# Optimization experiments

Measured on AMD Instinct MI355X. Metric: run time of the kernel, lower is better.

## Reference

```python
import jax, jax.numpy as jnp
import numpy as np

NUM_USERS = 100000
NUM_ITEMS = 50000
N_NODES = NUM_USERS + NUM_ITEMS
N_EDGES = 2400000
EMB = 64
BATCH = 4096
GCN_LAYERS = 3
TAU = 0.2
SSL_LAMBDA = 0.1
REG_LAMBDA = 1e-4


def setup_inputs() -> dict:
    key = jax.random.key(0)
    ks = jax.random.split(key, 8)
    user = jax.random.randint(ks[0], (BATCH,), 0, NUM_USERS, dtype=jnp.int32)
    pos_item = jax.random.randint(ks[1], (BATCH,), 0, NUM_ITEMS, dtype=jnp.int32)
    neg_item = jax.random.randint(ks[2], (BATCH,), 0, NUM_ITEMS, dtype=jnp.int32)
    # symmetric bipartite edges: user -> item and item -> user
    half = N_EDGES // 2
    src_u = jax.random.randint(ks[3], (half,), 0, NUM_USERS, dtype=jnp.int32)
    dst_i = jax.random.randint(ks[4], (half,), NUM_USERS, N_NODES, dtype=jnp.int32)
    adj_row = jnp.concatenate([src_u, dst_i])
    adj_col = jnp.concatenate([dst_i, src_u])
    # normalized-adjacency-like small positive values
    adj_val = jax.random.uniform(ks[5], (N_EDGES,), dtype=jnp.float32) * 0.01
    user_emb_w = jax.random.normal(ks[6], (NUM_USERS, EMB), dtype=jnp.float32) * 0.1
    item_emb_w = jax.random.normal(ks[7], (NUM_ITEMS, EMB), dtype=jnp.float32) * 0.1
    return {"user": user, "pos_item": pos_item, "neg_item": neg_item,
            "adj_row": adj_row, "adj_col": adj_col, "adj_val": adj_val,
            "user_emb_w": user_emb_w, "item_emb_w": item_emb_w}


def _aggregate(adj_row, adj_col, adj_val, user_emb_w, item_emb_w):
    emb = jnp.concatenate([user_emb_w, item_emb_w], axis=0)  # [N, d]
    acc = emb
    e = emb
    for _ in range(GCN_LAYERS):
        # sparse.mm(adj, e): gather columns, scale, scatter-add into rows
        e = jax.ops.segment_sum(adj_val[:, None] * e[adj_col], adj_row,
                                num_segments=N_NODES)
        acc = acc + e
    final = acc / (GCN_LAYERS + 1)  # mean over stacked layer outputs
    return final[:NUM_USERS], final[NUM_USERS:]


def reference(user, pos_item, neg_item, adj_row, adj_col, adj_val,
              user_emb_w, item_emb_w):
    user_all, item_all = _aggregate(adj_row, adj_col, adj_val,
                                    user_emb_w, item_emb_w)
    u = user_all[user]          # [B, d]
    pos = item_all[pos_item]    # [B, d]
    neg = item_all[neg_item]    # [B, d]
    # BPR loss
    pos_s = jnp.sum(u * pos, axis=-1)
    neg_s = jnp.sum(u * neg, axis=-1)
    bpr_loss = -jnp.mean(jax.nn.log_sigmoid(pos_s - neg_s))
    # L2 regularization
    b = u.shape[0]
    reg_loss = 0.5 * (jnp.sum(u * u) + jnp.sum(pos * pos) + jnp.sum(neg * neg)) / b
    reg_loss = reg_loss * REG_LAMBDA
    # neighbor-aggregate SSL (InfoNCE between user and its positive item)
    un = u / jnp.linalg.norm(u, axis=-1, keepdims=True)
    pn = pos / jnp.linalg.norm(pos, axis=-1, keepdims=True)
    logits = un @ pn.T / TAU                       # [B, B]
    pos_logit = jnp.diagonal(logits)
    na_loss = jnp.mean(jax.nn.logsumexp(logits, axis=1) - pos_logit) * SSL_LAMBDA
    return bpr_loss + reg_loss + na_loss
```

## Files before the change

### kernel.cpp

```cpp
#include <hip/hip_runtime.h>
#include <hip/hip_fp16.h>
#include <math.h>

#define NUM_USERS 100000
#define NUM_ITEMS 50000
#define N_NODES   150000
#define N_EDGES   2400000
#define HALF_E    (N_EDGES / 2)
#define EMB       64
#define BATCH     4096
#define TAU        0.2f
#define SSL_LAMBDA 0.1f
#define REG_LAMBDA 1e-4f

#define NB        293
#define BROWS     512
#define CAP       13632
#define BINA_BLK  512
#define PER_BLK   ((HALF_E + BINA_BLK - 1) / BINA_BLK)
#define EBUF_CAP  (2 * PER_BLK)
#define CAST_BLK  9375

__device__ __forceinline__ float wave_sum(float v) {
    #pragma unroll
    for (int m = 1; m < 64; m <<= 1) v += __shfl_xor(v, m, 64);
    return v;
}
__device__ __forceinline__ __half2 bits2h2(int b) {
    union { int i; __half2 h; } u; u.i = b; return u.h;
}
__device__ __forceinline__ int h22bits(__half2 h) {
    union { int i; __half2 h; } u; u.h = h; return u.i;
}
__device__ __forceinline__ float h2f(unsigned short s) {
    union { unsigned short s; __half h; } u; u.s = s; return __half2float(u.h);
}
__device__ __forceinline__ unsigned short f2h_bits(float x) {
    union { __half h; unsigned short s; } u; u.h = __float2half_rn(x); return u.s;
}

__global__ __launch_bounds__(256) void prep_kernel(
        const float4* __restrict__ uw4, const float4* __restrict__ iw4,
        uint2* __restrict__ h,
        const int* __restrict__ row, const int* __restrict__ col,
        const float* __restrict__ val,
        int* __restrict__ bucket_cursor, int2* __restrict__ arena) {
    __shared__ int hist[NB];
    __shared__ int lbase[NB];
    __shared__ int delta[NB];
    __shared__ int sm[256];
    __shared__ int2 ebuf[EBUF_CAP];
    const int t = threadIdx.x;
    size_t i = (size_t)blockIdx.x * 256 + t;
    const size_t tot = (size_t)N_NODES * EMB / 4;
    if (i < tot) {
        const size_t nu = (size_t)NUM_USERS * EMB / 4;
        float4 v = (i < nu) ? uw4[i] : iw4[i - nu];
        h[i] = make_uint2(h22bits(__floats2half2_rn(v.x, v.y)),
                          h22bits(__floats2half2_rn(v.z, v.w)));
    }
    if (blockIdx.x >= BINA_BLK) return;
    for (int k = t; k < NB; k += 256) hist[k] = 0;
    __syncthreads();
    const int beg = blockIdx.x * PER_BLK;
    const int end = min(beg + PER_BLK, HALF_E);
    for (int e = beg + t; e < end; e += 256) {
        int r = row[e], c = col[e];
        atomicAdd(&hist[r >> 9], 1);
        atomicAdd(&hist[c >> 9], 1);
    }
    __syncthreads();
    int v0 = (2 * t < NB) ? hist[2 * t] : 0;
    int v1 = (2 * t + 1 < NB) ? hist[2 * t + 1] : 0;
    int s = v0 + v1;
    sm[t] = s;
    __syncthreads();
    for (int m = 1; m < 256; m <<= 1) {
        int y = (t >= m) ? sm[t - m] : 0;
        __syncthreads();
        sm[t] += y;
        __syncthreads();
    }
    int excl = sm[t] - s;
    if (2 * t < NB) lbase[2 * t] = excl;
    if (2 * t + 1 < NB) lbase[2 * t + 1] = excl + v0;
    __syncthreads();
    for (int k = t; k < NB; k += 256) {
        int cnt = hist[k];
        int gb = cnt ? atomicAdd(&bucket_cursor[k], cnt) : 0;
        delta[k] = (k * CAP + gb) - lbase[k];
    }
    __syncthreads();
    for (int k = t; k < NB; k += 256) hist[k] = lbase[k];
    __syncthreads();
    for (int e = beg + t; e < end; e += 256) {
        int r = row[e], c = col[e];
        unsigned short h1 = f2h_bits(val[e]);
        unsigned short h2v = f2h_bits(val[e + HALF_E]);
        int b1 = r >> 9, b2 = c >> 9;
        int p1 = atomicAdd(&hist[b1], 1);
        int p2 = atomicAdd(&hist[b2], 1);
        ebuf[p1] = make_int2(c | ((r & 511) << 18), (b1 << 16) | h1);
        ebuf[p2] = make_int2(r | ((c & 511) << 18), (b2 << 16) | h2v);
    }
    __syncthreads();
    const int count = 2 * (end - beg);
    for (int k = t; k < count; k += 256) {
        int2 rec = ebuf[k];
        int b = rec.y >> 16;
        arena[k + delta[b]] = rec;
    }
}

__global__ __launch_bounds__(256) void bucket_scan(
        const int* __restrict__ bucket_cursor, int* __restrict__ bucket_base,
        int* __restrict__ rowptr) {
    __shared__ int sm[256];
    const int t = threadIdx.x;
    const int K = (NB + 255) / 256;
    int v[K], s = 0;
    #pragma unroll
    for (int j = 0; j < K; j++) {
        int idx = t * K + j;
        v[j] = (idx < NB) ? bucket_cursor[idx] : 0;
        s += v[j];
    }
    sm[t] = s;
    __syncthreads();
    for (int m = 1; m < 256; m <<= 1) {
        int y = (t >= m) ? sm[t - m] : 0;
        __syncthreads();
        sm[t] += y;
        __syncthreads();
    }
    int excl = sm[t] - s;
    #pragma unroll
    for (int j = 0; j < K; j++) {
        int idx = t * K + j;
        if (idx < NB) bucket_base[idx] = excl;
        excl += v[j];
    }
    if (t == 0) rowptr[N_NODES] = N_EDGES;
}

__global__ __launch_bounds__(1024) void bin_sort(
        const int* __restrict__ bucket_cursor, const int* __restrict__ bucket_base,
        const int2* __restrict__ arena,
        int* __restrict__ rowptr, int2* __restrict__ colval) {
    __shared__ int rcnt[BROWS];
    __shared__ int sm[256];
    const int bin = blockIdx.x;
    const int t = threadIdx.x;
    const int total = bucket_cursor[bin];
    const int count = min(total, CAP);
    const int gbase = bucket_base[bin];
    if (t < BROWS) rcnt[t] = 0;
    __syncthreads();
    for (int i = t; i < count; i += 1024) {
        int rx = arena[bin * CAP + i].x >> 18;
        atomicAdd(&rcnt[rx & 511], 1);
    }
    __syncthreads();
    int v0 = 0, v1 = 0, s = 0;
    if (t < 256) {
        v0 = rcnt[2 * t]; v1 = rcnt[2 * t + 1];
        s = v0 + v1;
        sm[t] = s;
    }
    __syncthreads();
    for (int m = 1; m < 256; m <<= 1) {
        int y = (t < 256 && t >= m) ? sm[t - m] : 0;
        __syncthreads();
        if (t < 256) sm[t] += y;
        __syncthreads();
    }
    if (t < 256) {
        int excl = sm[t] - s;
        rcnt[2 * t] = excl;
        rcnt[2 * t + 1] = excl + v0;
        int r0 = bin * BROWS + 2 * t;
        if (r0 < N_NODES) rowptr[r0] = gbase + excl;
        if (r0 + 1 < N_NODES) rowptr[r0 + 1] = gbase + excl + v0;
    }
    __syncthreads();
    for (int i = t; i < count; i += 1024) {
        int2 rec = arena[bin * CAP + i];
        int pos = atomicAdd(&rcnt[(rec.x >> 18) & 511], 1);
        unsigned int hv = (unsigned int)rec.y & 0xFFFFu;
        colval[gbase + pos] = make_int2(rec.x & 0x3FFFF, (int)(hv * 0x10001u));
    }
    for (int i = count + t; i < total; i += 1024)
        colval[gbase + i] = make_int2(0, 0);
}

__global__ __launch_bounds__(256) void spmm_csr(
        const int* __restrict__ rowptr, const int2* __restrict__ colval,
        const unsigned short* __restrict__ h_cur, unsigned short* __restrict__ h_next) {
    const int t = threadIdx.x;
    const int lane = t & 63;
    const int g = lane >> 3;
    const int l = lane & 7;
    int r = blockIdx.x * 4 + (t >> 6);
    if (r >= N_NODES) return;
    const int beg = rowptr[r], end = rowptr[r + 1];
    __half2 ac0 = __float2half2_rn(0.0f), ac1 = ac0, ac2 = ac0, ac3 = ac0;
    int e = beg + g;
    if (e < end) {
        int2 cv = colval[e];
        uint4 x = ((const uint4*)(h_cur + (size_t)cv.x * EMB))[l];
        e += 8;
        if (e < end) {
            int2 cv2 = colval[e];
            uint4 x2 = ((const uint4*)(h_cur + (size_t)cv2.x * EMB))[l];
            for (e += 8; e < end; e += 8) {
                int2 cv3 = colval[e];
                uint4 x3 = ((const uint4*)(h_cur + (size_t)cv3.x * EMB))[l];
                __half2 vv = bits2h2(cv.y);
                ac0 = __hfma2(vv, bits2h2(x.x), ac0);
                ac1 = __hfma2(vv, bits2h2(x.y), ac1);
                ac2 = __hfma2(vv, bits2h2(x.z), ac2);
                ac3 = __hfma2(vv, bits2h2(x.w), ac3);
                cv = cv2; x = x2; cv2 = cv3; x2 = x3;
            }
            __half2 vv = bits2h2(cv.y);
            ac0 = __hfma2(vv, bits2h2(x.x), ac0);
            ac1 = __hfma2(vv, bits2h2(x.y), ac1);
            ac2 = __hfma2(vv, bits2h2(x.z), ac2);
            ac3 = __hfma2(vv, bits2h2(x.w), ac3);
            cv = cv2; x = x2;
        }
        __half2 vv = bits2h2(cv.y);
        ac0 = __hfma2(vv, bits2h2(x.x), ac0);
        ac1 = __hfma2(vv, bits2h2(x.y), ac1);
        ac2 = __hfma2(vv, bits2h2(x.z), ac2);
        ac3 = __hfma2(vv, bits2h2(x.w), ac3);
    }
    int a0 = h22bits(ac0), a1 = h22bits(ac1), a2 = h22bits(ac2), a3 = h22bits(ac3);
    #pragma unroll
    for (int m = 8; m < 64; m <<= 1) {
        a0 = h22bits(__hadd2(bits2h2(a0), bits2h2(__shfl_xor(a0, m, 64))));
        a1 = h22bits(__hadd2(bits2h2(a1), bits2h2(__shfl_xor(a1, m, 64))));
        a2 = h22bits(__hadd2(bits2h2(a2), bits2h2(__shfl_xor(a2, m, 64))));
        a3 = h22bits(__hadd2(bits2h2(a3), bits2h2(__shfl_xor(a3, m, 64))));
    }
    if (g == 0)
        ((uint4*)(h_next + (size_t)r * EMB))[l] =
            make_uint4((unsigned)a0, (unsigned)a1, (unsigned)a2, (unsigned)a3);
}

__global__ __launch_bounds__(256) void spmm_sel(
        const int* __restrict__ rowptr, const int2* __restrict__ colval,
        const int* __restrict__ user, const int* __restrict__ pos,
        const int* __restrict__ neg,
        const unsigned short* __restrict__ h_cur, float* __restrict__ sel) {
    const int t = threadIdx.x;
    const int lane = t & 63;
    const int g = lane >> 3;
    const int l = lane & 7;
    int b = blockIdx.x * 4 + (t >> 6);
    if (b >= 3 * BATCH) return;
    int which = b / BATCH, bb = b - which * BATCH;
    int r = (which == 0) ? user[bb]
          : NUM_USERS + ((which == 1) ? pos[bb] : neg[bb]);
    const int beg = rowptr[r], end = rowptr[r + 1];
    __half2 ac0 = __float2half2_rn(0.0f), ac1 = ac0, ac2 = ac0, ac3 = ac0;
    int e = beg + g;
    if (e < end) {
        int2 cv = colval[e];
        uint4 x = ((const uint4*)(h_cur + (size_t)cv.x * EMB))[l];
        e += 8;
        if (e < end) {
            int2 cv2 = colval[e];
            uint4 x2 = ((const uint4*)(h_cur + (size_t)cv2.x * EMB))[l];
            for (e += 8; e < end; e += 8) {
                int2 cv3 = colval[e];
                uint4 x3 = ((const uint4*)(h_cur + (size_t)cv3.x * EMB))[l];
                __half2 vv = bits2h2(cv.y);
                ac0 = __hfma2(vv, bits2h2(x.x), ac0);
                ac1 = __hfma2(vv, bits2h2(x.y), ac1);
                ac2 = __hfma2(vv, bits2h2(x.z), ac2);
                ac3 = __hfma2(vv, bits2h2(x.w), ac3);
                cv = cv2; x = x2; cv2 = cv3; x2 = x3;
            }
            __half2 vv = bits2h2(cv.y);
            ac0 = __hfma2(vv, bits2h2(x.x), ac0);
            ac1 = __hfma2(vv, bits2h2(x.y), ac1);
            ac2 = __hfma2(vv, bits2h2(x.z), ac2);
            ac3 = __hfma2(vv, bits2h2(x.w), ac3);
            cv = cv2; x = x2;
        }
        __half2 vv = bits2h2(cv.y);
        ac0 = __hfma2(vv, bits2h2(x.x), ac0);
        ac1 = __hfma2(vv, bits2h2(x.y), ac1);
        ac2 = __hfma2(vv, bits2h2(x.z), ac2);
        ac3 = __hfma2(vv, bits2h2(x.w), ac3);
    }
    int a0 = h22bits(ac0), a1 = h22bits(ac1), a2 = h22bits(ac2), a3 = h22bits(ac3);
    #pragma unroll
    for (int m = 8; m < 64; m <<= 1) {
        a0 = h22bits(__hadd2(bits2h2(a0), bits2h2(__shfl_xor(a0, m, 64))));
        a1 = h22bits(__hadd2(bits2h2(a1), bits2h2(__shfl_xor(a1, m, 64))));
        a2 = h22bits(__hadd2(bits2h2(a2), bits2h2(__shfl_xor(a2, m, 64))));
        a3 = h22bits(__hadd2(bits2h2(a3), bits2h2(__shfl_xor(a3, m, 64))));
    }
    if (g == 0) {
        float2 f0 = __half22float2(bits2h2(a0));
        float2 f1 = __half22float2(bits2h2(a1));
        float2 f2 = __half22float2(bits2h2(a2));
        float2 f3 = __half22float2(bits2h2(a3));
        uint4 hx = ((const uint4*)(h_cur + (size_t)r * EMB))[l];
        float2 s0 = __half22float2(bits2h2((int)hx.x));
        float2 s1 = __half22float2(bits2h2((int)hx.y));
        float2 s2 = __half22float2(bits2h2((int)hx.z));
        float2 s3 = __half22float2(bits2h2((int)hx.w));
        float4* dst = (float4*)(sel + (size_t)b * EMB);
        dst[2 * l]     = make_float4(f0.x + s0.x, f0.y + s0.y, f1.x + s1.x, f1.y + s1.y);
        dst[2 * l + 1] = make_float4(f2.x + s2.x, f2.y + s2.y, f3.x + s3.x, f3.y + s3.y);
    }
}

__global__ __launch_bounds__(256) void batch_loss(
        const int* __restrict__ user, const int* __restrict__ pos,
        const int* __restrict__ neg,
        const float* __restrict__ uw, const float* __restrict__ iw,
        const unsigned short* __restrict__ h1,
        const float* __restrict__ sel,
        float* __restrict__ un, float* __restrict__ pn,
        float* __restrict__ diag,
        float* __restrict__ pbpr, float* __restrict__ preg) {
    __shared__ float lb[4], lr[4];
    const int t = threadIdx.x;
    const int lane = t & 63;
    const int w = t >> 6;
    int b = blockIdx.x * 4 + w;
    const float inv4 = 0.25f;
    int nu = user[b], np = pos[b], ng = neg[b];
    float u = (uw[(size_t)nu * EMB + lane]
             + h2f(h1[(size_t)nu * EMB + lane])
             + sel[(size_t)b * EMB + lane]) * inv4;
    float p = (iw[(size_t)np * EMB + lane]
             + h2f(h1[(size_t)(NUM_USERS + np) * EMB + lane])
             + sel[(size_t)(BATCH + b) * EMB + lane]) * inv4;
    float n = (iw[(size_t)ng * EMB + lane]
             + h2f(h1[(size_t)(NUM_USERS + ng) * EMB + lane])
             + sel[(size_t)(2 * BATCH + b) * EMB + lane]) * inv4;
    float pos_s = wave_sum(u * p);
    float neg_s = wave_sum(u * n);
    float uu = wave_sum(u * u);
    float pp = wave_sum(p * p);
    float nn = wave_sum(n * n);
    float ru = rsqrtf(uu), rp = rsqrtf(pp);
    un[(size_t)b * EMB + lane] = u * ru;
    pn[(size_t)b * EMB + lane] = p * rp;
    if (lane == 0) {
        diag[b] = pos_s * ru * rp * (1.0f / TAU);
        float d = pos_s - neg_s;
        float tt = -d;
        lb[w] = fmaxf(tt, 0.0f) + log1pf(expf(-fabsf(tt)));
        lr[w] = uu + pp + nn;
    }
    __syncthreads();
    if (t == 0) {
        pbpr[blockIdx.x] = lb[0] + lb[1] + lb[2] + lb[3];
        preg[blockIdx.x] = lr[0] + lr[1] + lr[2] + lr[3];
    }
}

#define TS 128
__global__ __launch_bounds__(256) void ssl_gemm(
        const float* __restrict__ un, const float* __restrict__ pn,
        float* __restrict__ rowsum_p) {
    __shared__ float ua[EMB][TS];
    __shared__ float pb[EMB][TS];
    const int t = threadIdx.x;
    const int it = blockIdx.x & 31, jt = blockIdx.x >> 5;
    const int i0 = it * TS;
    const int j0 = jt * TS;
    for (int x = t; x < TS * 16; x += 256) {
        int i = x & (TS - 1), d4 = x >> 7;
        float4 v = ((const float4*)(un + (size_t)(i0 + i) * EMB))[d4];
        ua[d4 * 4 + 0][i] = v.x; ua[d4 * 4 + 1][i] = v.y;
        ua[d4 * 4 + 2][i] = v.z; ua[d4 * 4 + 3][i] = v.w;
        float4 w = ((const float4*)(pn + (size_t)(j0 + i) * EMB))[d4];
        pb[d4 * 4 + 0][i] = w.x; pb[d4 * 4 + 1][i] = w.y;
        pb[d4 * 4 + 2][i] = w.z; pb[d4 * 4 + 3][i] = w.w;
    }
    __syncthreads();
    const int tx = t & 15, ty = t >> 4;
    float c[8][8];
    #pragma unroll
    for (int p = 0; p < 8; p++)
        #pragma unroll
        for (int q = 0; q < 8; q++) c[p][q] = 0.0f;
    for (int k = 0; k < EMB; k++) {
        float a[8], b[8];
        #pragma unroll
        for (int q = 0; q < 8; q++) { a[q] = ua[k][ty * 8 + q]; b[q] = pb[k][tx * 8 + q]; }
        #pragma unroll
        for (int p = 0; p < 8; p++)
            #pragma unroll
            for (int q = 0; q < 8; q++) c[p][q] = fmaf(a[p], b[q], c[p][q]);
    }
    float s[8];
    #pragma unroll
    for (int p = 0; p < 8; p++) {
        s[p] = 0.0f;
        #pragma unroll
        for (int q = 0; q < 8; q++) s[p] += __expf(c[p][q] * (1.0f / TAU));
    }
    #pragma unroll
    for (int m = 1; m < 16; m <<= 1)
        #pragma unroll
        for (int p = 0; p < 8; p++) s[p] += __shfl_xor(s[p], m, 64);
    if (tx == 0) {
        #pragma unroll
        for (int p = 0; p < 8; p++)
            rowsum_p[(size_t)jt * BATCH + i0 + ty * 8 + p] = s[p];
    }
}

__global__ __launch_bounds__(256) void finalize(
        const float* __restrict__ rowsum_p, const float* __restrict__ diag,
        const float* __restrict__ pbpr, const float* __restrict__ preg,
        float* __restrict__ out) {
    __shared__ float red[3][4];
    const int t = threadIdx.x;
    float sb = 0.0f, sr = 0.0f, ss = 0.0f;
    for (int i = t; i < BATCH / 4; i += 256) { sb += pbpr[i]; sr += preg[i]; }
    for (int i = t; i < BATCH; i += 256) {
        float rs = 0.0f;
        #pragma unroll
        for (int j = 0; j < 32; j++) rs += rowsum_p[(size_t)j * BATCH + i];
        ss += logf(rs) - diag[i];
    }
    sb = wave_sum(sb); sr = wave_sum(sr); ss = wave_sum(ss);
    const int w = t >> 6;
    if ((t & 63) == 0) { red[0][w] = sb; red[1][w] = sr; red[2][w] = ss; }
    __syncthreads();
    if (t == 0) {
        float bpr_sum = red[0][0] + red[0][1] + red[0][2] + red[0][3];
        float reg_sum = red[1][0] + red[1][1] + red[1][2] + red[1][3];
        float ssl_sum = red[2][0] + red[2][1] + red[2][2] + red[2][3];
        float bpr = bpr_sum * (1.0f / BATCH);
        float reg = 0.5f * reg_sum * (1.0f / BATCH) * REG_LAMBDA;
        float ssl = ssl_sum * (1.0f / BATCH) * SSL_LAMBDA;
        out[0] = bpr + reg + ssl;
    }
}

extern "C" void kernel_launch(void* const* d_in, const int* in_sizes, int n_in,
                              void* d_out, int out_size, void* d_ws, size_t ws_size,
                              hipStream_t stream) {
    const int*   user    = (const int*)d_in[0];
    const int*   pos     = (const int*)d_in[1];
    const int*   neg     = (const int*)d_in[2];
    const int*   adj_row = (const int*)d_in[3];
    const int*   adj_col = (const int*)d_in[4];
    const float* adj_val = (const float*)d_in[5];
    const float* user_w  = (const float*)d_in[6];
    const float* item_w  = (const float*)d_in[7];
    float* out = (float*)d_out;

    unsigned short* hA = (unsigned short*)d_ws;
    unsigned short* hB = hA + (size_t)N_NODES * EMB;
    float* buf1   = (float*)d_ws + (size_t)N_NODES * EMB;
    float* sel    = buf1 + (size_t)N_NODES * EMB;
    float* un     = sel  + (size_t)3 * BATCH * EMB;
    float* pn     = un   + (size_t)BATCH * EMB;
    float* diag   = pn   + (size_t)BATCH * EMB;
    float* rowsum_p = diag + BATCH;
    float* pbpr   = rowsum_p + 32 * BATCH;
    float* preg   = pbpr + 1024;
    int*   rowptr = (int*)(preg + 1024);
    int*   bucket_cursor = rowptr + 150016;
    int*   bucket_base   = bucket_cursor + 512;
    int2*  colval = (int2*)(bucket_base + 512);
    int2*  arena  = (int2*)buf1;

    hipMemsetAsync(bucket_cursor, 0, 512 * sizeof(int), stream);

    dim3 blk(256);

    prep_kernel<<<CAST_BLK, blk, 0, stream>>>((const float4*)user_w,
                                              (const float4*)item_w, (uint2*)hA,
                                              adj_row, adj_col, adj_val,
                                              bucket_cursor, arena);
    bucket_scan<<<1, blk, 0, stream>>>(bucket_cursor, bucket_base, rowptr);
    bin_sort<<<NB, dim3(1024), 0, stream>>>(bucket_cursor, bucket_base, arena,
                                            rowptr, colval);

    spmm_csr<<<(N_NODES + 3) / 4, blk, 0, stream>>>(rowptr, colval, hA, hB);
    spmm_csr<<<(N_NODES + 3) / 4, blk, 0, stream>>>(rowptr, colval, hB, hA);
    spmm_sel<<<(3 * BATCH + 3) / 4, blk, 0, stream>>>(rowptr, colval, user, pos,
                                                      neg, hA, sel);

    batch_loss<<<BATCH / 4, blk, 0, stream>>>(user, pos, neg, user_w, item_w,
                                              hB, sel, un, pn, diag, pbpr, preg);
    ssl_gemm<<<(BATCH / TS) * (BATCH / TS), blk, 0, stream>>>(un, pn, rowsum_p);
    finalize<<<1, blk, 0, stream>>>(rowsum_p, diag, pbpr, preg, out);
}
```

Baseline: 317.5 us.

## Use fp16 MFMA for SSL logits and split cast from edge binning

Normalized user and positive embeddings are now stored in fp16. The fp32 FMA tiled GEMM for the InfoNCE logits is replaced by a wave-level MFMA 16x16x32 kernel that fuses the exp row-sum and splits columns four ways. The embedding cast kernel is also separated from the edge histogram/scatter kernel, and it zeroes the bucket cursors itself, so the memset call is removed. The aim is cheaper SSL logits and fewer launches, at the cost of fp16 rounding in the similarity values.

```diff
diff --git a/kernel.cpp b/kernel.cpp
--- a/kernel.cpp
+++ b/kernel.cpp
@@ -20,6 +20,7 @@
 #define PER_BLK   ((HALF_E + BINA_BLK - 1) / BINA_BLK)
 #define EBUF_CAP  (2 * PER_BLK)
 #define CAST_BLK  9375
+#define JSPLIT    4
 
 __device__ __forceinline__ float wave_sum(float v) {
     #pragma unroll
@@ -38,10 +39,24 @@
 __device__ __forceinline__ unsigned short f2h_bits(float x) {
     union { __half h; unsigned short s; } u; u.h = __float2half_rn(x); return u.s;
 }
-
-__global__ __launch_bounds__(256) void prep_kernel(
+typedef _Float16 half8 __attribute__((ext_vector_type(8)));
+typedef float f32x4 __attribute__((ext_vector_type(4)));
+
+__global__ __launch_bounds__(256) void cast_h0(
         const float4* __restrict__ uw4, const float4* __restrict__ iw4,
-        uint2* __restrict__ h,
+        uint2* __restrict__ h, int* __restrict__ bucket_cursor) {
+    const int t = threadIdx.x;
+    if (blockIdx.x < 2) bucket_cursor[blockIdx.x * 256 + t] = 0;
+    size_t i = (size_t)blockIdx.x * 256 + t;
+    const size_t tot = (size_t)N_NODES * EMB / 4;
+    if (i >= tot) return;
+    const size_t nu = (size_t)NUM_USERS * EMB / 4;
+    float4 v = (i < nu) ? uw4[i] : iw4[i - nu];
+    h[i] = make_uint2(h22bits(__floats2half2_rn(v.x, v.y)),
+                      h22bits(__floats2half2_rn(v.z, v.w)));
+}
+
+__global__ __launch_bounds__(256) void bin_scatter(
         const int* __restrict__ row, const int* __restrict__ col,
         const float* __restrict__ val,
         int* __restrict__ bucket_cursor, int2* __restrict__ arena) {
@@ -51,15 +66,6 @@
     __shared__ int sm[256];
     __shared__ int2 ebuf[EBUF_CAP];
     const int t = threadIdx.x;
-    size_t i = (size_t)blockIdx.x * 256 + t;
-    const size_t tot = (size_t)N_NODES * EMB / 4;
-    if (i < tot) {
-        const size_t nu = (size_t)NUM_USERS * EMB / 4;
-        float4 v = (i < nu) ? uw4[i] : iw4[i - nu];
-        h[i] = make_uint2(h22bits(__floats2half2_rn(v.x, v.y)),
-                          h22bits(__floats2half2_rn(v.z, v.w)));
-    }
-    if (blockIdx.x >= BINA_BLK) return;
     for (int k = t; k < NB; k += 256) hist[k] = 0;
     __syncthreads();
     const int beg = blockIdx.x * PER_BLK;
@@ -325,7 +331,7 @@
         const float* __restrict__ uw, const float* __restrict__ iw,
         const unsigned short* __restrict__ h1,
         const float* __restrict__ sel,
-        float* __restrict__ un, float* __restrict__ pn,
+        unsigned short* __restrict__ unh, unsigned short* __restrict__ pnh,
         float* __restrict__ diag,
         float* __restrict__ pbpr, float* __restrict__ preg) {
     __shared__ float lb[4], lr[4];
@@ -350,8 +356,8 @@
     float pp = wave_sum(p * p);
     float nn = wave_sum(n * n);
     float ru = rsqrtf(uu), rp = rsqrtf(pp);
-    un[(size_t)b * EMB + lane] = u * ru;
-    pn[(size_t)b * EMB + lane] = p * rp;
+    unh[(size_t)b * EMB + lane] = f2h_bits(u * ru);
+    pnh[(size_t)b * EMB + lane] = f2h_bits(p * rp);
     if (lane == 0) {
         diag[b] = pos_s * ru * rp * (1.0f / TAU);
         float d = pos_s - neg_s;
@@ -366,56 +372,40 @@
     }
 }
 
-#define TS 128
-__global__ __launch_bounds__(256) void ssl_gemm(
-        const float* __restrict__ un, const float* __restrict__ pn,
+__global__ __launch_bounds__(256) void ssl_mfma(
+        const unsigned short* __restrict__ unh, const unsigned short* __restrict__ pnh,
         float* __restrict__ rowsum_p) {
-    __shared__ float ua[EMB][TS];
-    __shared__ float pb[EMB][TS];
-    const int t = threadIdx.x;
-    const int it = blockIdx.x & 31, jt = blockIdx.x >> 5;
-    const int i0 = it * TS;
-    const int j0 = jt * TS;
-    for (int x = t; x < TS * 16; x += 256) {
-        int i = x & (TS - 1), d4 = x >> 7;
-        float4 v = ((const float4*)(un + (size_t)(i0 + i) * EMB))[d4];
-        ua[d4 * 4 + 0][i] = v.x; ua[d4 * 4 + 1][i] = v.y;
-        ua[d4 * 4 + 2][i] = v.z; ua[d4 * 4 + 3][i] = v.w;
-        float4 w = ((const float4*)(pn + (size_t)(j0 + i) * EMB))[d4];
-        pb[d4 * 4 + 0][i] = w.x; pb[d4 * 4 + 1][i] = w.y;
-        pb[d4 * 4 + 2][i] = w.z; pb[d4 * 4 + 3][i] = w.w;
-    }
-    __syncthreads();
-    const int tx = t & 15, ty = t >> 4;
-    float c[8][8];
-    #pragma unroll
-    for (int p = 0; p < 8; p++)
-        #pragma unroll
-        for (int q = 0; q < 8; q++) c[p][q] = 0.0f;
-    for (int k = 0; k < EMB; k++) {
-        float a[8], b[8];
-        #pragma unroll
-        for (int q = 0; q < 8; q++) { a[q] = ua[k][ty * 8 + q]; b[q] = pb[k][tx * 8 + q]; }
-        #pragma unroll
-        for (int p = 0; p < 8; p++)
-            #pragma unroll
-            for (int q = 0; q < 8; q++) c[p][q] = fmaf(a[p], b[q], c[p][q]);
-    }
-    float s[8];
-    #pragma unroll
-    for (int p = 0; p < 8; p++) {
-        s[p] = 0.0f;
-        #pragma unroll
-        for (int q = 0; q < 8; q++) s[p] += __expf(c[p][q] * (1.0f / TAU));
-    }
-    #pragma unroll
-    for (int m = 1; m < 16; m <<= 1)
-        #pragma unroll
-        for (int p = 0; p < 8; p++) s[p] += __shfl_xor(s[p], m, 64);
-    if (tx == 0) {
-        #pragma unroll
-        for (int p = 0; p < 8; p++)
-            rowsum_p[(size_t)jt * BATCH + i0 + ty * 8 + p] = s[p];
+    const int t = threadIdx.x;
+    const int lane = t & 63;
+    const int idx = lane & 15, quad = lane >> 4;
+    int job = blockIdx.x * 4 + (t >> 6);
+    int it = job & 255, js = job >> 8;
+    const int i0 = it * 16;
+    half8 a0 = *(const half8*)(unh + (size_t)(i0 + idx) * EMB + quad * 8);
+    half8 a1 = *(const half8*)(unh + (size_t)(i0 + idx) * EMB + 32 + quad * 8);
+    float rs0 = 0.0f, rs1 = 0.0f, rs2 = 0.0f, rs3 = 0.0f;
+    for (int jt = 0; jt < 64; jt++) {
+        int j0 = js * 1024 + jt * 16;
+        half8 b0 = *(const half8*)(pnh + (size_t)(j0 + idx) * EMB + quad * 8);
+        half8 b1 = *(const half8*)(pnh + (size_t)(j0 + idx) * EMB + 32 + quad * 8);
+        f32x4 c = {0.0f, 0.0f, 0.0f, 0.0f};
+        c = __builtin_amdgcn_mfma_f32_16x16x32_f16(a0, b0, c, 0, 0, 0);
+        c = __builtin_amdgcn_mfma_f32_16x16x32_f16(a1, b1, c, 0, 0, 0);
+        rs0 += __expf(c[0] * (1.0f / TAU));
+        rs1 += __expf(c[1] * (1.0f / TAU));
+        rs2 += __expf(c[2] * (1.0f / TAU));
+        rs3 += __expf(c[3] * (1.0f / TAU));
+    }
+    #pragma unroll
+    for (int m = 1; m < 16; m <<= 1) {
+        rs0 += __shfl_xor(rs0, m, 64);
+        rs1 += __shfl_xor(rs1, m, 64);
+        rs2 += __shfl_xor(rs2, m, 64);
+        rs3 += __shfl_xor(rs3, m, 64);
+    }
+    if (idx == 0) {
+        float* dst = rowsum_p + (size_t)js * BATCH + i0 + quad * 4;
+        dst[0] = rs0; dst[1] = rs1; dst[2] = rs2; dst[3] = rs3;
     }
 }
 
@@ -430,7 +420,7 @@
     for (int i = t; i < BATCH; i += 256) {
         float rs = 0.0f;
         #pragma unroll
-        for (int j = 0; j < 32; j++) rs += rowsum_p[(size_t)j * BATCH + i];
+        for (int j = 0; j < JSPLIT; j++) rs += rowsum_p[(size_t)j * BATCH + i];
         ss += logf(rs) - diag[i];
     }
     sb = wave_sum(sb); sr = wave_sum(sr); ss = wave_sum(ss);
@@ -465,11 +455,11 @@
     unsigned short* hB = hA + (size_t)N_NODES * EMB;
     float* buf1   = (float*)d_ws + (size_t)N_NODES * EMB;
     float* sel    = buf1 + (size_t)N_NODES * EMB;
-    float* un     = sel  + (size_t)3 * BATCH * EMB;
-    float* pn     = un   + (size_t)BATCH * EMB;
-    float* diag   = pn   + (size_t)BATCH * EMB;
+    unsigned short* unh = (unsigned short*)(sel + (size_t)3 * BATCH * EMB);
+    unsigned short* pnh = unh + (size_t)BATCH * EMB;
+    float* diag   = (float*)(pnh + (size_t)BATCH * EMB);
     float* rowsum_p = diag + BATCH;
-    float* pbpr   = rowsum_p + 32 * BATCH;
+    float* pbpr   = rowsum_p + JSPLIT * BATCH;
     float* preg   = pbpr + 1024;
     int*   rowptr = (int*)(preg + 1024);
     int*   bucket_cursor = rowptr + 150016;
@@ -477,13 +467,12 @@
     int2*  colval = (int2*)(bucket_base + 512);
     int2*  arena  = (int2*)buf1;
 
-    hipMemsetAsync(bucket_cursor, 0, 512 * sizeof(int), stream);
-
     dim3 blk(256);
 
-    prep_kernel<<<CAST_BLK, blk, 0, stream>>>((const float4*)user_w,
-                                              (const float4*)item_w, (uint2*)hA,
-                                              adj_row, adj_col, adj_val,
+    cast_h0<<<CAST_BLK, blk, 0, stream>>>((const float4*)user_w,
+                                          (const float4*)item_w, (uint2*)hA,
+                                          bucket_cursor);
+    bin_scatter<<<BINA_BLK, blk, 0, stream>>>(adj_row, adj_col, adj_val,
                                               bucket_cursor, arena);
     bucket_scan<<<1, blk, 0, stream>>>(bucket_cursor, bucket_base, rowptr);
     bin_sort<<<NB, dim3(1024), 0, stream>>>(bucket_cursor, bucket_base, arena,
@@ -495,7 +484,7 @@
                                                       neg, hA, sel);
 
     batch_loss<<<BATCH / 4, blk, 0, stream>>>(user, pos, neg, user_w, item_w,
-                                              hB, sel, un, pn, diag, pbpr, preg);
-    ssl_gemm<<<(BATCH / TS) * (BATCH / TS), blk, 0, stream>>>(un, pn, rowsum_p);
+                                              hB, sel, unh, pnh, diag, pbpr, preg);
+    ssl_mfma<<<256, blk, 0, stream>>>(unh, pnh, rowsum_p);
     finalize<<<1, blk, 0, stream>>>(rowsum_p, diag, pbpr, preg, out);
 }
```

Measured after the change: 309.5 us. 2.5% less time.
